# Optimization experiments

Hardware: AMD Instinct MI355X
Metric: run time of the kernel (lower is better)

The kernel has to match this reference:

```python
import jax, jax.numpy as jnp
import numpy as np

NEG = -1e9
LRELU_ALPHA = 0.2  # tf.nn.leaky_relu default


def setup_inputs() -> dict:
    key = jax.random.key(0)
    k = jax.random.split(key, 6)
    B, N, F_in, F_out = 1, 8192, 256, 64
    x = jax.random.normal(k[0], (B, N, F_in), dtype=jnp.float32)
    # sparse adjacency as additive bias: ~32 neighbors/node on average
    u = jax.random.uniform(k[1], (B, N, N), dtype=jnp.float32)
    adj = jnp.where(u < 32.0 / N, 0.0, NEG).astype(jnp.float32)
    W = jax.random.normal(k[2], (F_in, F_out), dtype=jnp.float32) * (1.0 / np.sqrt(F_in))
    a1 = jax.random.normal(k[3], (F_out, 1), dtype=jnp.float32) * (1.0 / np.sqrt(F_out))
    a2 = jax.random.normal(k[4], (F_out, 1), dtype=jnp.float32) * (1.0 / np.sqrt(F_out))
    b1 = jnp.zeros((1,), dtype=jnp.float32)
    b2 = jnp.zeros((1,), dtype=jnp.float32)
    bias = jnp.zeros((F_out,), dtype=jnp.float32)
    return {"x": x, "adj": adj, "W": W, "a1": a1, "b1": b1, "a2": a2, "b2": b2, "bias": bias}


def reference(x, adj, W, a1, b1, a2, b2, bias):
    # conv1 (kernel_size=1, no bias) == per-node linear projection
    fts = jnp.einsum('bnf,fo->bno', x, W)            # [B, N, F_out]
    f1 = jnp.einsum('bno,oi->bni', fts, a1) + b1     # [B, N, 1]
    f2 = jnp.einsum('bno,oi->bni', fts, a2) + b2     # [B, N, 1]
    logits = f1 + jnp.swapaxes(f2, 1, 2)             # [B, N, N] additive scores
    scores = jax.nn.leaky_relu(logits, LRELU_ALPHA) + adj
    coefs = jax.nn.softmax(scores, axis=-1)          # [B, N, N]
    vals = jnp.einsum('bnm,bmo->bno', coefs, fts) + bias
    return jax.nn.elu(vals)
```

## Files before the change

kernel.cpp:

```cpp
#include <hip/hip_runtime.h>
#include <hip/hip_bf16.h>
#include <cstdint>

#define N_NODES 8192
#define F_IN    256
#define F_OUT   64
#define ALPHA   0.2f

__global__ __launch_bounds__(256) void k_proj(const float* __restrict__ x,
                                              const float* __restrict__ W,
                                              float* __restrict__ fts) {
    __shared__ __align__(16) float ws[F_IN][F_OUT];
    const int t = threadIdx.x;
    const int row0 = blockIdx.x * 32;

    {
        const float4* W4 = (const float4*)W;
        float4* S4 = (float4*)&ws[0][0];
        #pragma unroll
        for (int i = 0; i < 16; ++i) S4[i * 256 + t] = W4[i * 256 + t];
    }
    __syncthreads();

    const int rg = t >> 4;
    const int cg = t & 15;
    const int r0 = row0 + rg * 2;
    const int c0 = cg * 4;

    float4 acc0 = {0.f,0.f,0.f,0.f}, acc1 = {0.f,0.f,0.f,0.f};
    const float4* xr0 = (const float4*)(x + (size_t)r0 * F_IN);
    const float4* xr1 = (const float4*)(x + (size_t)(r0 + 1) * F_IN);

    #pragma unroll 4
    for (int kq = 0; kq < 64; ++kq) {
        const float4 xa = xr0[kq];
        const float4 xb = xr1[kq];
        const float4 w0 = *(const float4*)&ws[kq*4+0][c0];
        const float4 w1 = *(const float4*)&ws[kq*4+1][c0];
        const float4 w2 = *(const float4*)&ws[kq*4+2][c0];
        const float4 w3 = *(const float4*)&ws[kq*4+3][c0];
        acc0.x += xa.x*w0.x + xa.y*w1.x + xa.z*w2.x + xa.w*w3.x;
        acc0.y += xa.x*w0.y + xa.y*w1.y + xa.z*w2.y + xa.w*w3.y;
        acc0.z += xa.x*w0.z + xa.y*w1.z + xa.z*w2.z + xa.w*w3.z;
        acc0.w += xa.x*w0.w + xa.y*w1.w + xa.z*w2.w + xa.w*w3.w;
        acc1.x += xb.x*w0.x + xb.y*w1.x + xb.z*w2.x + xb.w*w3.x;
        acc1.y += xb.x*w0.y + xb.y*w1.y + xb.z*w2.y + xb.w*w3.y;
        acc1.z += xb.x*w0.z + xb.y*w1.z + xb.z*w2.z + xb.w*w3.z;
        acc1.w += xb.x*w0.w + xb.y*w1.w + xb.z*w2.w + xb.w*w3.w;
    }
    float* o = fts + (size_t)r0 * F_OUT + c0;
    *(float4*)o          = acc0;
    *(float4*)(o + F_OUT) = acc1;
}

__global__ __launch_bounds__(256) void k_f12(const float* __restrict__ fts,
                                             const float* __restrict__ a1,
                                             const float* __restrict__ b1,
                                             const float* __restrict__ a2,
                                             const float* __restrict__ b2,
                                             float* __restrict__ f1,
                                             float* __restrict__ f2) {
    const int row = blockIdx.x * blockDim.x + threadIdx.x;
    const float4* v4 = (const float4*)(fts + (size_t)row * F_OUT);
    const float4* A1 = (const float4*)a1;
    const float4* A2 = (const float4*)a2;
    float s1 = 0.f, s2 = 0.f;
    #pragma unroll
    for (int q = 0; q < 16; ++q) {
        const float4 v = v4[q], u1 = A1[q], u2 = A2[q];
        s1 += v.x*u1.x + v.y*u1.y + v.z*u1.z + v.w*u1.w;
        s2 += v.x*u2.x + v.y*u2.y + v.z*u2.z + v.w*u2.w;
    }
    f1[row] = s1 + b1[0];
    f2[row] = s2 + b2[0];
}

__global__ __launch_bounds__(256) void k_attn(const float* __restrict__ adj,
                                              const float* __restrict__ fts,
                                              const float* __restrict__ f1,
                                              const float* __restrict__ f2,
                                              const float* __restrict__ bias,
                                              float* __restrict__ out) {
    __shared__ __align__(16) float p_lds[N_NODES];
    __shared__ float red_max[4], red_sum[4];
    __shared__ float opart[4][F_OUT];

    const int row  = blockIdx.x;
    const int t    = threadIdx.x;
    const int lane = t & 63;
    const int w    = t >> 6;

    const float4* arow = (const float4*)(adj + (size_t)row * N_NODES);
    const float4* f24  = (const float4*)f2;
    const float   f1r  = f1[row];

    float s[32];
    float m = -3.0e38f;
    #pragma unroll
    for (int c = 0; c < 8; ++c) {
        const int q = c * 256 + t;
        const float4 a  = arow[q];
        const float4 fv = f24[q];
        float4 sv;
        { const float l = f1r + fv.x; sv.x = fmaxf(l, ALPHA * l) + a.x; }
        { const float l = f1r + fv.y; sv.y = fmaxf(l, ALPHA * l) + a.y; }
        { const float l = f1r + fv.z; sv.z = fmaxf(l, ALPHA * l) + a.z; }
        { const float l = f1r + fv.w; sv.w = fmaxf(l, ALPHA * l) + a.w; }
        s[4*c+0] = sv.x; s[4*c+1] = sv.y; s[4*c+2] = sv.z; s[4*c+3] = sv.w;
        m = fmaxf(m, fmaxf(fmaxf(sv.x, sv.y), fmaxf(sv.z, sv.w)));
    }
    #pragma unroll
    for (int off = 32; off >= 1; off >>= 1)
        m = fmaxf(m, __shfl_xor(m, off, 64));
    if (lane == 0) red_max[w] = m;
    __syncthreads();
    m = fmaxf(fmaxf(red_max[0], red_max[1]), fmaxf(red_max[2], red_max[3]));

    float lsum = 0.f;
    #pragma unroll
    for (int c = 0; c < 8; ++c) {
        const int q = c * 256 + t;
        float4 pv;
        pv.x = __expf(s[4*c+0] - m);
        pv.y = __expf(s[4*c+1] - m);
        pv.z = __expf(s[4*c+2] - m);
        pv.w = __expf(s[4*c+3] - m);
        lsum += pv.x + pv.y + pv.z + pv.w;
        ((float4*)p_lds)[q] = pv;
    }
    #pragma unroll
    for (int off = 32; off >= 1; off >>= 1)
        lsum += __shfl_xor(lsum, off, 64);
    if (lane == 0) red_sum[w] = lsum;
    __syncthreads();
    const float sum = red_sum[0] + red_sum[1] + red_sum[2] + red_sum[3];

    float acc = 0.f;
    const int jbase0 = w * 2048;
    for (int it = 0; it < 32; ++it) {
        const int jb = jbase0 + it * 64;
        const float p = p_lds[jb + lane];
        unsigned long long mk = __ballot(p > 0.f);
        while (mk) {
            const int b = __ffsll(mk) - 1;
            mk &= mk - 1;
            const float pb = __shfl(p, b, 64);
            acc += pb * fts[(size_t)(jb + b) * F_OUT + lane];
        }
    }
    opart[w][lane] = acc;
    __syncthreads();

    if (w == 0) {
        const float tot = opart[0][lane] + opart[1][lane] + opart[2][lane] + opart[3][lane];
        const float v = tot / sum + bias[lane];
        out[(size_t)row * F_OUT + lane] = (v > 0.f) ? v : expm1f(v);
    }
}

extern "C" void kernel_launch(void* const* d_in, const int* in_sizes, int n_in,
                              void* d_out, int out_size, void* d_ws, size_t ws_size,
                              hipStream_t stream) {
    const float* x    = (const float*)d_in[0];
    const float* adj  = (const float*)d_in[1];
    const float* W    = (const float*)d_in[2];
    const float* a1   = (const float*)d_in[3];
    const float* b1   = (const float*)d_in[4];
    const float* a2   = (const float*)d_in[5];
    const float* b2   = (const float*)d_in[6];
    const float* bias = (const float*)d_in[7];
    float* out = (float*)d_out;

    float* fts = (float*)d_ws;
    float* f1  = fts + (size_t)N_NODES * F_OUT;
    float* f2  = f1 + N_NODES;

    k_proj<<<N_NODES / 32, 256, 0, stream>>>(x, W, fts);
    k_f12 <<<N_NODES / 256, 256, 0, stream>>>(fts, a1, b1, a2, b2, f1, f2);
    k_attn<<<N_NODES, 256, 0, stream>>>(adj, fts, f1, f2, bias, out);
}
```

Baseline: 396.9 us.

## Fuse f1/f2 into projection and use single-pass online softmax in attention

The f1/f2 dot products move into the projection kernel, computed with a 16-lane shuffle reduction, so one launch and a reread of fts are gone; the projection now handles 16 rows per block instead of 32. The attention kernel becomes a single pass with a per-wave online softmax: it drops the 32 KB LDS probability buffer and the block-wide max barrier and merges per-wave partial sums at the end with rescaling. This cuts LDS use, which should raise occupancy, and removes a sync. In exchange it adds a wave-wide max reduction per chunk and processes 4 columns per ballot bit with extra conditional branches.

```diff
diff --git a/kernel.cpp b/kernel.cpp
--- a/kernel.cpp
+++ b/kernel.cpp
@@ -1,18 +1,23 @@
 #include <hip/hip_runtime.h>
-#include <hip/hip_bf16.h>
 #include <cstdint>
 
 #define N_NODES 8192
 #define F_IN    256
 #define F_OUT   64
 #define ALPHA   0.2f
+#define ROWS_PB 16
 
 __global__ __launch_bounds__(256) void k_proj(const float* __restrict__ x,
                                               const float* __restrict__ W,
-                                              float* __restrict__ fts) {
+                                              const float* __restrict__ a1,
+                                              const float* __restrict__ b1,
+                                              const float* __restrict__ a2,
+                                              const float* __restrict__ b2,
+                                              float* __restrict__ fts,
+                                              float* __restrict__ f1,
+                                              float* __restrict__ f2) {
     __shared__ __align__(16) float ws[F_IN][F_OUT];
     const int t = threadIdx.x;
-    const int row0 = blockIdx.x * 32;
 
     {
         const float4* W4 = (const float4*)W;
@@ -22,57 +27,41 @@
     }
     __syncthreads();
 
-    const int rg = t >> 4;
-    const int cg = t & 15;
-    const int r0 = row0 + rg * 2;
-    const int c0 = cg * 4;
+    const int rg  = t >> 4;
+    const int cg  = t & 15;
+    const int row = blockIdx.x * ROWS_PB + rg;
+    const int c0  = cg * 4;
 
-    float4 acc0 = {0.f,0.f,0.f,0.f}, acc1 = {0.f,0.f,0.f,0.f};
-    const float4* xr0 = (const float4*)(x + (size_t)r0 * F_IN);
-    const float4* xr1 = (const float4*)(x + (size_t)(r0 + 1) * F_IN);
+    float4 acc = {0.f, 0.f, 0.f, 0.f};
+    const float4* xr = (const float4*)(x + (size_t)row * F_IN);
 
     #pragma unroll 4
     for (int kq = 0; kq < 64; ++kq) {
-        const float4 xa = xr0[kq];
-        const float4 xb = xr1[kq];
+        const float4 xa = xr[kq];
         const float4 w0 = *(const float4*)&ws[kq*4+0][c0];
         const float4 w1 = *(const float4*)&ws[kq*4+1][c0];
         const float4 w2 = *(const float4*)&ws[kq*4+2][c0];
         const float4 w3 = *(const float4*)&ws[kq*4+3][c0];
-        acc0.x += xa.x*w0.x + xa.y*w1.x + xa.z*w2.x + xa.w*w3.x;
-        acc0.y += xa.x*w0.y + xa.y*w1.y + xa.z*w2.y + xa.w*w3.y;
-        acc0.z += xa.x*w0.z + xa.y*w1.z + xa.z*w2.z + xa.w*w3.z;
-        acc0.w += xa.x*w0.w + xa.y*w1.w + xa.z*w2.w + xa.w*w3.w;
-        acc1.x += xb.x*w0.x + xb.y*w1.x + xb.z*w2.x + xb.w*w3.x;
-        acc1.y += xb.x*w0.y + xb.y*w1.y + xb.z*w2.y + xb.w*w3.y;
-        acc1.z += xb.x*w0.z + xb.y*w1.z + xb.z*w2.z + xb.w*w3.z;
-        acc1.w += xb.x*w0.w + xb.y*w1.w + xb.z*w2.w + xb.w*w3.w;
+        acc.x += xa.x*w0.x + xa.y*w1.x + xa.z*w2.x + xa.w*w3.x;
+        acc.y += xa.x*w0.y + xa.y*w1.y + xa.z*w2.y + xa.w*w3.y;
+        acc.z += xa.x*w0.z + xa.y*w1.z + xa.z*w2.z + xa.w*w3.z;
+        acc.w += xa.x*w0.w + xa.y*w1.w + xa.z*w2.w + xa.w*w3.w;
     }
-    float* o = fts + (size_t)r0 * F_OUT + c0;
-    *(float4*)o          = acc0;
-    *(float4*)(o + F_OUT) = acc1;
-}
+    *(float4*)(fts + (size_t)row * F_OUT + c0) = acc;
 
-__global__ __launch_bounds__(256) void k_f12(const float* __restrict__ fts,
-                                             const float* __restrict__ a1,
-                                             const float* __restrict__ b1,
-                                             const float* __restrict__ a2,
-                                             const float* __restrict__ b2,
-                                             float* __restrict__ f1,
-                                             float* __restrict__ f2) {
-    const int row = blockIdx.x * blockDim.x + threadIdx.x;
-    const float4* v4 = (const float4*)(fts + (size_t)row * F_OUT);
-    const float4* A1 = (const float4*)a1;
-    const float4* A2 = (const float4*)a2;
-    float s1 = 0.f, s2 = 0.f;
+    const float4 u1 = ((const float4*)a1)[cg];
+    const float4 u2 = ((const float4*)a2)[cg];
+    float s1 = acc.x*u1.x + acc.y*u1.y + acc.z*u1.z + acc.w*u1.w;
+    float s2 = acc.x*u2.x + acc.y*u2.y + acc.z*u2.z + acc.w*u2.w;
     #pragma unroll
-    for (int q = 0; q < 16; ++q) {
-        const float4 v = v4[q], u1 = A1[q], u2 = A2[q];
-        s1 += v.x*u1.x + v.y*u1.y + v.z*u1.z + v.w*u1.w;
-        s2 += v.x*u2.x + v.y*u2.y + v.z*u2.z + v.w*u2.w;
+    for (int off = 8; off >= 1; off >>= 1) {
+        s1 += __shfl_xor(s1, off, 64);
+        s2 += __shfl_xor(s2, off, 64);
     }
-    f1[row] = s1 + b1[0];
-    f2[row] = s2 + b2[0];
+    if (cg == 0) {
+        f1[row] = s1 + b1[0];
+        f2[row] = s2 + b2[0];
+    }
 }
 
 __global__ __launch_bounds__(256) void k_attn(const float* __restrict__ adj,
@@ -81,79 +70,83 @@
                                               const float* __restrict__ f2,
                                               const float* __restrict__ bias,
                                               float* __restrict__ out) {
-    __shared__ __align__(16) float p_lds[N_NODES];
-    __shared__ float red_max[4], red_sum[4];
-    __shared__ float opart[4][F_OUT];
+    __shared__ float wmax[4], wsum[4];
+    __shared__ __align__(16) float wacc[4][F_OUT];
 
     const int row  = blockIdx.x;
     const int t    = threadIdx.x;
     const int lane = t & 63;
     const int w    = t >> 6;
 
-    const float4* arow = (const float4*)(adj + (size_t)row * N_NODES);
-    const float4* f24  = (const float4*)f2;
-    const float   f1r  = f1[row];
+    const float   f1r   = f1[row];
+    const float4* arow4 = (const float4*)(adj + (size_t)row * N_NODES);
+    const float4* f24   = (const float4*)f2;
 
-    float s[32];
-    float m = -3.0e38f;
-    #pragma unroll
-    for (int c = 0; c < 8; ++c) {
-        const int q = c * 256 + t;
-        const float4 a  = arow[q];
-        const float4 fv = f24[q];
-        float4 sv;
-        { const float l = f1r + fv.x; sv.x = fmaxf(l, ALPHA * l) + a.x; }
-        { const float l = f1r + fv.y; sv.y = fmaxf(l, ALPHA * l) + a.y; }
-        { const float l = f1r + fv.z; sv.z = fmaxf(l, ALPHA * l) + a.z; }
-        { const float l = f1r + fv.w; sv.w = fmaxf(l, ALPHA * l) + a.w; }
-        s[4*c+0] = sv.x; s[4*c+1] = sv.y; s[4*c+2] = sv.z; s[4*c+3] = sv.w;
-        m = fmaxf(m, fmaxf(fmaxf(sv.x, sv.y), fmaxf(sv.z, sv.w)));
+    float m = -1.0e30f, lsum = 0.f, acc = 0.f;
+
+    #pragma unroll 2
+    for (int i = 0; i < 8; ++i) {
+        const int jq = w * 512 + i * 64 + lane;
+        const float4 a  = arow4[jq];
+        const float4 fv = f24[jq];
+
+        float s0, s1, s2, s3;
+        { const float l = f1r + fv.x; s0 = fmaxf(l, ALPHA * l) + a.x; }
+        { const float l = f1r + fv.y; s1 = fmaxf(l, ALPHA * l) + a.y; }
+        { const float l = f1r + fv.z; s2 = fmaxf(l, ALPHA * l) + a.z; }
+        { const float l = f1r + fv.w; s3 = fmaxf(l, ALPHA * l) + a.w; }
+
+        float cm = fmaxf(fmaxf(s0, s1), fmaxf(s2, s3));
+        #pragma unroll
+        for (int off = 32; off >= 1; off >>= 1)
+            cm = fmaxf(cm, __shfl_xor(cm, off, 64));
+
+        if (cm > m) {
+            const float fac = __expf(m - cm);
+            acc *= fac; lsum *= fac; m = cm;
+        }
+
+        const float p0 = __expf(s0 - m);
+        const float p1 = __expf(s1 - m);
+        const float p2 = __expf(s2 - m);
+        const float p3 = __expf(s3 - m);
+        const float ps = (p0 + p1) + (p2 + p3);
+        lsum += ps;
+
+        unsigned long long mk = __ballot(ps > 0.f);
+        const int jb = w * 2048 + i * 256;
+        while (mk) {
+            const int b = __ffsll(mk) - 1;
+            mk &= mk - 1;
+            const float q0 = __shfl(p0, b, 64);
+            const float q1 = __shfl(p1, b, 64);
+            const float q2 = __shfl(p2, b, 64);
+            const float q3 = __shfl(p3, b, 64);
+            const float* fr = fts + (size_t)(jb + 4 * b) * F_OUT + lane;
+            if (q0 > 0.f) acc += q0 * fr[0];
+            if (q1 > 0.f) acc += q1 * fr[F_OUT];
+            if (q2 > 0.f) acc += q2 * fr[2 * F_OUT];
+            if (q3 > 0.f) acc += q3 * fr[3 * F_OUT];
+        }
     }
-    #pragma unroll
-    for (int off = 32; off >= 1; off >>= 1)
-        m = fmaxf(m, __shfl_xor(m, off, 64));
-    if (lane == 0) red_max[w] = m;
-    __syncthreads();
-    m = fmaxf(fmaxf(red_max[0], red_max[1]), fmaxf(red_max[2], red_max[3]));
 
-    float lsum = 0.f;
-    #pragma unroll
-    for (int c = 0; c < 8; ++c) {
-        const int q = c * 256 + t;
-        float4 pv;
-        pv.x = __expf(s[4*c+0] - m);
-        pv.y = __expf(s[4*c+1] - m);
-        pv.z = __expf(s[4*c+2] - m);
-        pv.w = __expf(s[4*c+3] - m);
-        lsum += pv.x + pv.y + pv.z + pv.w;
-        ((float4*)p_lds)[q] = pv;
-    }
     #pragma unroll
     for (int off = 32; off >= 1; off >>= 1)
         lsum += __shfl_xor(lsum, off, 64);
-    if (lane == 0) red_sum[w] = lsum;
-    __syncthreads();
-    const float sum = red_sum[0] + red_sum[1] + red_sum[2] + red_sum[3];
-
-    float acc = 0.f;
-    const int jbase0 = w * 2048;
-    for (int it = 0; it < 32; ++it) {
-        const int jb = jbase0 + it * 64;
-        const float p = p_lds[jb + lane];
-        unsigned long long mk = __ballot(p > 0.f);
-        while (mk) {
-            const int b = __ffsll(mk) - 1;
-            mk &= mk - 1;
-            const float pb = __shfl(p, b, 64);
-            acc += pb * fts[(size_t)(jb + b) * F_OUT + lane];
-        }
-    }
-    opart[w][lane] = acc;
+    if (lane == 0) { wmax[w] = m; wsum[w] = lsum; }
+    wacc[w][lane] = acc;
     __syncthreads();
 
     if (w == 0) {
-        const float tot = opart[0][lane] + opart[1][lane] + opart[2][lane] + opart[3][lane];
-        const float v = tot / sum + bias[lane];
+        const float M  = fmaxf(fmaxf(wmax[0], wmax[1]), fmaxf(wmax[2], wmax[3]));
+        const float e0 = __expf(wmax[0] - M);
+        const float e1 = __expf(wmax[1] - M);
+        const float e2 = __expf(wmax[2] - M);
+        const float e3 = __expf(wmax[3] - M);
+        const float tot = wacc[0][lane]*e0 + wacc[1][lane]*e1
+                        + wacc[2][lane]*e2 + wacc[3][lane]*e3;
+        const float den = wsum[0]*e0 + wsum[1]*e1 + wsum[2]*e2 + wsum[3]*e3;
+        const float v = tot / den + bias[lane];
         out[(size_t)row * F_OUT + lane] = (v > 0.f) ? v : expm1f(v);
     }
 }
@@ -175,7 +168,6 @@
     float* f1  = fts + (size_t)N_NODES * F_OUT;
     float* f2  = f1 + N_NODES;
 
-    k_proj<<<N_NODES / 32, 256, 0, stream>>>(x, W, fts);
-    k_f12 <<<N_NODES / 256, 256, 0, stream>>>(fts, a1, b1, a2, b2, f1, f2);
+    k_proj<<<N_NODES / ROWS_PB, 256, 0, stream>>>(x, W, a1, b1, a2, b2, fts, f1, f2);
     k_attn<<<N_NODES, 256, 0, stream>>>(adj, fts, f1, f2, bias, out);
 }
```

Measured after the change: 1.005 ms. +153.4%, slower.
